# Kernel tuning notes

Hardware: AMD Instinct MI355X
Metric: run time of the kernel (lower is better)

## Reference

```python
import jax, jax.numpy as jnp
import numpy as np

B, N, DIM = 4, 2048, 1024
HEADS, DIM_HEAD = 16, 64
INNER = HEADS * DIM_HEAD


def setup_inputs() -> dict:
    key = jax.random.key(0)
    kx, kw = jax.random.split(key)
    x = jax.random.normal(kx, (B, N, DIM), dtype=jnp.float32)
    # Dense kernel [in_features, out_features], no bias
    w_qkv = jax.random.normal(kw, (DIM, 3 * INNER), dtype=jnp.float32) * (DIM ** -0.5)
    return {"x": x, "w_qkv": w_qkv}


def reference(x, w_qkv):
    scale = DIM_HEAD ** (-0.5)
    qkv = jnp.einsum('bnc,cf->bnf', x, w_qkv)  # [B, N, 3*INNER]
    q, k, v = jnp.split(qkv, 3, axis=-1)
    # 'b n (h d) -> b h n d'
    def to_heads(t):
        return t.reshape(B, N, HEADS, DIM_HEAD).transpose(0, 2, 1, 3)
    q, k, v = map(to_heads, (q, k, v))
    dots = jnp.einsum('bhid,bhjd->bhij', q, k) * scale  # [B, H, N, N]
    attn = jax.nn.softmax(dots, axis=-1)
    out = jnp.einsum('bhij,bhjd->bhid', attn, v)  # [B, H, N, D]
    # 'b h n d -> b n (h d)'
    return out.transpose(0, 2, 1, 3).reshape(B, N, INNER)
```

## Files before the change

### kernel.cpp

```cpp
#include <hip/hip_runtime.h>
#include <hip/hip_bf16.h>
#include <math.h>

typedef __bf16 bf16x2 __attribute__((ext_vector_type(2)));
typedef __bf16 bf16x4 __attribute__((ext_vector_type(4)));
typedef __bf16 bf16x8 __attribute__((ext_vector_type(8)));
typedef float f32x4 __attribute__((ext_vector_type(4)));
typedef float f32x16 __attribute__((ext_vector_type(16)));

#define MFMA16(a, b, c) __builtin_amdgcn_mfma_f32_16x16x32_bf16(a, b, c, 0, 0, 0)
#define MFMA32(a, b, c) __builtin_amdgcn_mfma_f32_32x32x16_bf16(a, b, c, 0, 0, 0)
#define QSCALE 0.1803368801111204f

__device__ __forceinline__ void gload_lds16(const __bf16* g, __bf16* l) {
  __builtin_amdgcn_global_load_lds((const __attribute__((address_space(1))) void*)g,
                                   (__attribute__((address_space(3))) void*)l,
                                   16, 0, 0);
}

__global__ __launch_bounds__(256) void convert_x(const float* __restrict__ in,
                                                 __bf16* __restrict__ out) {
  int i = blockIdx.x * 256 + threadIdx.x;
  float4 v = ((const float4*)in)[i];
  bf16x4 o = {(__bf16)v.x, (__bf16)v.y, (__bf16)v.z, (__bf16)v.w};
  *(bf16x4*)&out[i * 4] = o;
}

__global__ __launch_bounds__(256) void transpose_w(const float* __restrict__ W,
                                                   __bf16* __restrict__ Wt) {
  __shared__ __bf16 tile[64][65];
  const int bx = blockIdx.x;
  const int by = blockIdx.y;
  const int t = threadIdx.x;
  const int lr = t >> 6;
  const int lc = t & 63;
  const float sc = (bx < 16) ? QSCALE : 1.0f;
#pragma unroll
  for (int i = 0; i < 16; ++i) {
    int r = lr + i * 4;
    tile[r][lc] = (__bf16)(W[(size_t)(by * 64 + r) * 3072 + bx * 64 + lc] * sc);
  }
  __syncthreads();
#pragma unroll
  for (int i = 0; i < 16; ++i) {
    int r = lr + i * 4;
    Wt[(size_t)(bx * 64 + r) * 1024 + by * 64 + lc] = tile[lc][r];
  }
}

__global__ __launch_bounds__(256) void gemm_qkv(const __bf16* __restrict__ X,
                                                const __bf16* __restrict__ Wt,
                                                __bf16* __restrict__ QK,
                                                __bf16* __restrict__ Vt) {
  __shared__ __bf16 As[128 * 32];
  __shared__ __bf16 Bs[128 * 32];
  const int t = threadIdx.x;
  const int lane = t & 63;
  const int wave = t >> 6;
  const int quad = lane >> 4;
  const int l16 = lane & 15;
  const int n0 = blockIdx.x * 128;
  const int m0 = blockIdx.y * 128;
  const int wm = (wave & 1) * 64;
  const int wn = (wave >> 1) * 64;

  const __bf16* Ag = &X[(size_t)(m0 + wave * 16 + (lane >> 2)) * 1024 + (lane & 3) * 8];
  const __bf16* Bg = &Wt[(size_t)(n0 + wave * 16 + (lane >> 2)) * 1024 + (lane & 3) * 8];
  __bf16* As0 = &As[wave * 512];
  __bf16* As1 = &As[2048 + wave * 512];
  __bf16* Bs0 = &Bs[wave * 512];
  __bf16* Bs1 = &Bs[2048 + wave * 512];

  f32x4 acc[4][4] = {};

  for (int k0 = 0; k0 < 1024; k0 += 32) {
    gload_lds16(Ag + k0, As0);
    gload_lds16(Ag + (size_t)64 * 1024 + k0, As1);
    gload_lds16(Bg + k0, Bs0);
    gload_lds16(Bg + (size_t)64 * 1024 + k0, Bs1);
    __syncthreads();

    bf16x8 af[4], bf[4];
#pragma unroll
    for (int mi = 0; mi < 4; ++mi)
      af[mi] = *(const bf16x8*)&As[(wm + mi * 16 + l16) * 32 + quad * 8];
#pragma unroll
    for (int ni = 0; ni < 4; ++ni)
      bf[ni] = *(const bf16x8*)&Bs[(wn + ni * 16 + l16) * 32 + quad * 8];
#pragma unroll
    for (int mi = 0; mi < 4; ++mi)
#pragma unroll
      for (int ni = 0; ni < 4; ++ni)
        acc[mi][ni] = MFMA16(af[mi], bf[ni], acc[mi][ni]);
    __syncthreads();
  }

  if (n0 < 2048) {
#pragma unroll
    for (int mi = 0; mi < 4; ++mi)
#pragma unroll
      for (int ni = 0; ni < 4; ++ni)
#pragma unroll
        for (int r = 0; r < 4; ++r) {
          int row = m0 + wm + mi * 16 + quad * 4 + r;
          int col = n0 + wn + ni * 16 + l16;
          QK[(size_t)row * 2048 + col] = (__bf16)acc[mi][ni][r];
        }
  } else {
#pragma unroll
    for (int mi = 0; mi < 4; ++mi)
#pragma unroll
      for (int ni = 0; ni < 4; ++ni) {
        int v = n0 + wn + ni * 16 + l16 - 2048;
        int hh = v >> 6, d = v & 63;
        int row0 = m0 + wm + mi * 16 + quad * 4;
        int bb = row0 >> 11, key = row0 & 2047;
        bf16x4 pk = {(__bf16)acc[mi][ni][0], (__bf16)acc[mi][ni][1],
                     (__bf16)acc[mi][ni][2], (__bf16)acc[mi][ni][3]};
        *(bf16x4*)&Vt[((size_t)(bb * 16 + hh) * 64 + d) * 2048 + key] = pk;
      }
  }
}

#define AT_LD 72

__global__ __launch_bounds__(256) void attn(const __bf16* __restrict__ QK,
                                            const __bf16* __restrict__ Vt,
                                            float* __restrict__ Out) {
  const int t = threadIdx.x;
  const int lane = t & 63;
  const int wave = t >> 6;
  const int l31 = lane & 31;
  const int half = lane >> 5;

  const int flat = blockIdx.x + (blockIdx.y << 4) + (blockIdx.z << 8);
  const int xcd = flat & 7;
  const int idx = flat >> 3;
  const int bh = xcd * 8 + (idx >> 4);
  const int qb = idx & 15;
  const int b = bh >> 4;
  const int h = bh & 15;
  const int q0w = qb * 128 + wave * 32;

  const size_t base = (size_t)b * 2048 * 2048;
  const __bf16* Qb = QK + base + h * 64;
  const __bf16* Kb = QK + base + 1024 + h * 64;
  const __bf16* Vtb = Vt + (size_t)(b * 16 + h) * 64 * 2048;

  __shared__ __bf16 Ks[64 * AT_LD];
  __shared__ __bf16 Vs[64 * AT_LD];

  bf16x8 qf[4];
#pragma unroll
  for (int dc = 0; dc < 4; ++dc)
    qf[dc] = *(const bf16x8*)&Qb[(size_t)(q0w + l31) * 2048 + dc * 16 + half * 8];

  f32x16 o[2] = {};
  float lsum = 0.0f;

  const int srow = t >> 2;
  const int sc = (t & 3) * 16;
  const int prow = (srow & 51) | ((srow & 4) << 1) | ((srow & 8) >> 1);

  for (int kv0 = 0; kv0 < 2048; kv0 += 64) {
    bf16x8 k0v = *(const bf16x8*)&Kb[(size_t)(kv0 + srow) * 2048 + sc];
    bf16x8 k1v = *(const bf16x8*)&Kb[(size_t)(kv0 + srow) * 2048 + sc + 8];
    bf16x8 v0v = *(const bf16x8*)&Vtb[(size_t)srow * 2048 + kv0 + sc];
    bf16x8 v1v = *(const bf16x8*)&Vtb[(size_t)srow * 2048 + kv0 + sc + 8];
    __syncthreads();
    *(bf16x8*)&Ks[prow * AT_LD + sc] = k0v;
    *(bf16x8*)&Ks[prow * AT_LD + sc + 8] = k1v;
    *(bf16x8*)&Vs[srow * AT_LD + sc] = v0v;
    *(bf16x8*)&Vs[srow * AT_LD + sc + 8] = v1v;
    __syncthreads();

    bf16x8 pf[4];
#pragma unroll
    for (int kt = 0; kt < 2; ++kt) {
      f32x16 c = {};
#pragma unroll
      for (int dc = 0; dc < 4; ++dc) {
        bf16x8 kf = *(const bf16x8*)&Ks[(kt * 32 + l31) * AT_LD + dc * 16 + half * 8];
        c = MFMA32(kf, qf[dc], c);
      }
#pragma unroll
      for (int kkl = 0; kkl < 2; ++kkl) {
        bf16x8 f;
#pragma unroll
        for (int j = 0; j < 8; ++j) {
          float e = __builtin_amdgcn_exp2f(c[8 * kkl + 4 * (j >> 2) + (j & 3)]);
          lsum += e;
          f[j] = (__bf16)e;
        }
        pf[kt * 2 + kkl] = f;
      }
    }

#pragma unroll
    for (int dt = 0; dt < 2; ++dt)
#pragma unroll
      for (int kk = 0; kk < 4; ++kk) {
        bf16x8 vf = *(const bf16x8*)&Vs[(dt * 32 + l31) * AT_LD + kk * 16 + half * 8];
        o[dt] = MFMA32(pf[kk], vf, o[dt]);
      }
  }

  lsum += __shfl_xor(lsum, 32);
  float inv = 1.0f / lsum;

  float iv[16];
#pragma unroll
  for (int r = 0; r < 16; ++r)
    iv[r] = __shfl(inv, (r & 3) + 8 * (r >> 2) + 4 * half);

#pragma unroll
  for (int dt = 0; dt < 2; ++dt)
#pragma unroll
    for (int r = 0; r < 16; ++r) {
      int qr = (r & 3) + 8 * (r >> 2) + 4 * half;
      Out[(size_t)(b * 2048 + q0w + qr) * 1024 + h * 64 + dt * 32 + l31] =
          o[dt][r] * iv[r];
    }
}

extern "C" void kernel_launch(void* const* d_in, const int* in_sizes, int n_in,
                              void* d_out, int out_size, void* d_ws, size_t ws_size,
                              hipStream_t stream) {
  const float* x = (const float*)d_in[0];
  const float* w = (const float*)d_in[1];
  float* out = (float*)d_out;

  __bf16* Wt = (__bf16*)d_ws;
  __bf16* QK = Wt + (size_t)3072 * 1024;
  __bf16* Xb = QK + (size_t)8192 * 2048;
  __bf16* Vtr = Xb + (size_t)8192 * 1024;

  convert_x<<<8192, 256, 0, stream>>>(x, Xb);
  transpose_w<<<dim3(48, 16), 256, 0, stream>>>(w, Wt);
  gemm_qkv<<<dim3(24, 64), 256, 0, stream>>>(Xb, Wt, QK, Vtr);
  attn<<<dim3(16, 16, 4), 256, 0, stream>>>(QK, Vtr, out);
}
```

Before: 234.3 us.

## Double-buffer QKV GEMM with 256x128 tiles, swizzled LDS, interleaved loads

Rewrites the QKV projection GEMM to use 512-thread blocks with 256x128 output tiles and a K-step of 64. The LDS is double-buffered so the next tile's global-to-LDS loads are issued between MFMA groups, and only one barrier is needed per step. An XOR swizzle reduces LDS bank conflicts, and s_setprio is raised around the MFMA groups. The cost is 96KB of dynamic LDS per block, which limits occupancy, plus added scheduling complexity.

```diff
diff --git a/kernel.cpp b/kernel.cpp
--- a/kernel.cpp
+++ b/kernel.cpp
@@ -48,51 +48,125 @@
   }
 }
 
-__global__ __launch_bounds__(256) void gemm_qkv(const __bf16* __restrict__ X,
-                                                const __bf16* __restrict__ Wt,
-                                                __bf16* __restrict__ QK,
-                                                __bf16* __restrict__ Vt) {
-  __shared__ __bf16 As[128 * 32];
-  __shared__ __bf16 Bs[128 * 32];
+#define GSLOT 24576
+
+__global__ __launch_bounds__(512, 2) void gemm_qkv(const __bf16* __restrict__ X,
+                                                   const __bf16* __restrict__ Wt,
+                                                   __bf16* __restrict__ QK,
+                                                   __bf16* __restrict__ Vt) {
+  extern __shared__ __bf16 lds[];
   const int t = threadIdx.x;
   const int lane = t & 63;
-  const int wave = t >> 6;
+  const int w = t >> 6;
   const int quad = lane >> 4;
   const int l16 = lane & 15;
   const int n0 = blockIdx.x * 128;
-  const int m0 = blockIdx.y * 128;
-  const int wm = (wave & 1) * 64;
-  const int wn = (wave >> 1) * 64;
-
-  const __bf16* Ag = &X[(size_t)(m0 + wave * 16 + (lane >> 2)) * 1024 + (lane & 3) * 8];
-  const __bf16* Bg = &Wt[(size_t)(n0 + wave * 16 + (lane >> 2)) * 1024 + (lane & 3) * 8];
-  __bf16* As0 = &As[wave * 512];
-  __bf16* As1 = &As[2048 + wave * 512];
-  __bf16* Bs0 = &Bs[wave * 512];
-  __bf16* Bs1 = &Bs[2048 + wave * 512];
+  const int m0 = blockIdx.y * 256;
+  const int wm = (w >> 1) * 64;
+  const int wn = (w & 1) * 64;
+  const int sw = (lane & 12) << 2;
+  const int colSw = ((lane & 7) << 3) ^ ((lane & 32) >> 1) ^ ((w & 1) << 5);
+
+  const __bf16* Asrc = &X[(size_t)(m0 + w * 8 + (lane >> 3)) * 1024 + colSw];
+  const __bf16* Bsrc = &Wt[(size_t)(n0 + w * 8 + (lane >> 3)) * 1024 + colSw];
+  const int dstAw = w * 8 * 64;
+  const int dstBw = 16384 + w * 8 * 64;
 
   f32x4 acc[4][4] = {};
 
-  for (int k0 = 0; k0 < 1024; k0 += 32) {
-    gload_lds16(Ag + k0, As0);
-    gload_lds16(Ag + (size_t)64 * 1024 + k0, As1);
-    gload_lds16(Bg + k0, Bs0);
-    gload_lds16(Bg + (size_t)64 * 1024 + k0, Bs1);
-    __syncthreads();
-
-    bf16x8 af[4], bf[4];
-#pragma unroll
-    for (int mi = 0; mi < 4; ++mi)
-      af[mi] = *(const bf16x8*)&As[(wm + mi * 16 + l16) * 32 + quad * 8];
+  {
+    __bf16* T = lds;
+#pragma unroll
+    for (int a = 0; a < 4; ++a)
+      gload_lds16(Asrc + (size_t)a * 64 * 1024, T + dstAw + a * 4096);
+#pragma unroll
+    for (int b = 0; b < 2; ++b)
+      gload_lds16(Bsrc + (size_t)b * 64 * 1024, T + dstBw + b * 4096);
+    asm volatile("s_waitcnt vmcnt(0)" ::: "memory");
+    __builtin_amdgcn_sched_barrier(0);
+    __builtin_amdgcn_s_barrier();
+    __builtin_amdgcn_sched_barrier(0);
+  }
+
+  for (int c = 0; c < 16; ++c) {
+    __bf16* S = lds + (c & 1) * GSLOT;
+    __bf16* T = lds + ((c & 1) ^ 1) * GSLOT;
+    const size_t kn = (size_t)(c + 1) * 64;
+    const bool st = c < 15;
+
+    if (st) {
+      gload_lds16(Asrc + kn, T + dstAw);
+      gload_lds16(Asrc + (size_t)64 * 1024 + kn, T + dstAw + 4096);
+      gload_lds16(Asrc + (size_t)128 * 1024 + kn, T + dstAw + 2 * 4096);
+    }
+    bf16x8 af0[2][2], af1[2][2], bf[4][2];
+#pragma unroll
+    for (int mi = 0; mi < 2; ++mi)
+#pragma unroll
+      for (int kk = 0; kk < 2; ++kk)
+        af0[mi][kk] = *(const bf16x8*)&S[(wm + mi * 16 + l16) * 64 +
+                                         ((kk * 32 + quad * 8) ^ sw)];
 #pragma unroll
     for (int ni = 0; ni < 4; ++ni)
-      bf[ni] = *(const bf16x8*)&Bs[(wn + ni * 16 + l16) * 32 + quad * 8];
-#pragma unroll
-    for (int mi = 0; mi < 4; ++mi)
-#pragma unroll
-      for (int ni = 0; ni < 4; ++ni)
-        acc[mi][ni] = MFMA16(af[mi], bf[ni], acc[mi][ni]);
-    __syncthreads();
+#pragma unroll
+      for (int kk = 0; kk < 2; ++kk)
+        bf[ni][kk] = *(const bf16x8*)&S[16384 + (wn + ni * 16 + l16) * 64 +
+                                        ((kk * 32 + quad * 8) ^ sw)];
+    __builtin_amdgcn_s_setprio(1);
+#pragma unroll
+    for (int mi = 0; mi < 2; ++mi)
+#pragma unroll
+      for (int ni = 0; ni < 2; ++ni)
+#pragma unroll
+        for (int kk = 0; kk < 2; ++kk)
+          acc[mi][ni] = MFMA16(af0[mi][kk], bf[ni][kk], acc[mi][ni]);
+    __builtin_amdgcn_s_setprio(0);
+
+    if (st) {
+      gload_lds16(Asrc + (size_t)192 * 1024 + kn, T + dstAw + 3 * 4096);
+      gload_lds16(Bsrc + kn, T + dstBw);
+      gload_lds16(Bsrc + (size_t)64 * 1024 + kn, T + dstBw + 4096);
+    }
+    __builtin_amdgcn_s_setprio(1);
+#pragma unroll
+    for (int mi = 0; mi < 2; ++mi)
+#pragma unroll
+      for (int ni = 0; ni < 2; ++ni)
+#pragma unroll
+        for (int kk = 0; kk < 2; ++kk)
+          acc[mi][2 + ni] = MFMA16(af0[mi][kk], bf[2 + ni][kk], acc[mi][2 + ni]);
+    __builtin_amdgcn_s_setprio(0);
+
+#pragma unroll
+    for (int mi = 0; mi < 2; ++mi)
+#pragma unroll
+      for (int kk = 0; kk < 2; ++kk)
+        af1[mi][kk] = *(const bf16x8*)&S[(wm + (2 + mi) * 16 + l16) * 64 +
+                                         ((kk * 32 + quad * 8) ^ sw)];
+    __builtin_amdgcn_s_setprio(1);
+#pragma unroll
+    for (int mi = 0; mi < 2; ++mi)
+#pragma unroll
+      for (int ni = 0; ni < 2; ++ni)
+#pragma unroll
+        for (int kk = 0; kk < 2; ++kk)
+          acc[2 + mi][2 + ni] = MFMA16(af1[mi][kk], bf[2 + ni][kk], acc[2 + mi][2 + ni]);
+    __builtin_amdgcn_s_setprio(0);
+
+    __builtin_amdgcn_s_setprio(1);
+#pragma unroll
+    for (int mi = 0; mi < 2; ++mi)
+#pragma unroll
+      for (int ni = 0; ni < 2; ++ni)
+#pragma unroll
+        for (int kk = 0; kk < 2; ++kk)
+          acc[2 + mi][ni] = MFMA16(af1[mi][kk], bf[ni][kk], acc[2 + mi][ni]);
+    __builtin_amdgcn_s_setprio(0);
+
+    asm volatile("s_waitcnt vmcnt(0) lgkmcnt(0)" ::: "memory");
+    __builtin_amdgcn_sched_barrier(0);
+    __builtin_amdgcn_s_barrier();
+    __builtin_amdgcn_sched_barrier(0);
   }
 
   if (n0 < 2048) {
@@ -235,8 +309,16 @@
   __bf16* Xb = QK + (size_t)8192 * 2048;
   __bf16* Vtr = Xb + (size_t)8192 * 1024;
 
+  static bool attr_done = false;
+  if (!attr_done) {
+    (void)hipFuncSetAttribute((const void*)gemm_qkv,
+                              hipFuncAttributeMaxDynamicSharedMemorySize,
+                              2 * GSLOT * (int)sizeof(__bf16));
+    attr_done = true;
+  }
+
   convert_x<<<8192, 256, 0, stream>>>(x, Xb);
   transpose_w<<<dim3(48, 16), 256, 0, stream>>>(w, Wt);
-  gemm_qkv<<<dim3(24, 64), 256, 0, stream>>>(Xb, Wt, QK, Vtr);
+  gemm_qkv<<<dim3(24, 32), 512, 2 * GSLOT * sizeof(__bf16), stream>>>(Xb, Wt, QK, Vtr);
   attn<<<dim3(16, 16, 4), 256, 0, stream>>>(QK, Vtr, out);
 }
```

After: 239.0 us. No clear change (+2.0%).

## Pipeline QKV GEMM with 4-stage LDS ring buffer and 256x128 tiles

Applied to the files above, without the earlier changes.

Restructures the QKV projection GEMM to use 512-thread blocks computing 256x128 tiles, with a 4-deep ring of LDS buffers filled by direct global-to-LDS loads three K-steps ahead. Explicit vmcnt waits and barriers replace the per-iteration sync pairs, and MFMA sections get raised wave priority. The goal is to hide global load latency behind matrix math and improve reuse of the weight tile. It needs 96KB of dynamic LDS, which limits blocks per CU, and it relies on hand-tuned wait counts.

```diff
diff --git a/kernel.cpp b/kernel.cpp
--- a/kernel.cpp
+++ b/kernel.cpp
@@ -48,52 +48,90 @@
   }
 }
 
-__global__ __launch_bounds__(256) void gemm_qkv(const __bf16* __restrict__ X,
-                                                const __bf16* __restrict__ Wt,
-                                                __bf16* __restrict__ QK,
-                                                __bf16* __restrict__ Vt) {
-  __shared__ __bf16 As[128 * 32];
-  __shared__ __bf16 Bs[128 * 32];
+#define GTOT_B 98304
+
+__global__ __launch_bounds__(512, 2) void gemm_qkv(const __bf16* __restrict__ X,
+                                                   const __bf16* __restrict__ Wt,
+                                                   __bf16* __restrict__ QK,
+                                                   __bf16* __restrict__ Vt) {
+  extern __shared__ __bf16 lds[];
   const int t = threadIdx.x;
   const int lane = t & 63;
-  const int wave = t >> 6;
+  const int w = t >> 6;
   const int quad = lane >> 4;
   const int l16 = lane & 15;
   const int n0 = blockIdx.x * 128;
-  const int m0 = blockIdx.y * 128;
-  const int wm = (wave & 1) * 64;
-  const int wn = (wave >> 1) * 64;
-
-  const __bf16* Ag = &X[(size_t)(m0 + wave * 16 + (lane >> 2)) * 1024 + (lane & 3) * 8];
-  const __bf16* Bg = &Wt[(size_t)(n0 + wave * 16 + (lane >> 2)) * 1024 + (lane & 3) * 8];
-  __bf16* As0 = &As[wave * 512];
-  __bf16* As1 = &As[2048 + wave * 512];
-  __bf16* Bs0 = &Bs[wave * 512];
-  __bf16* Bs1 = &Bs[2048 + wave * 512];
+  const int m0 = blockIdx.y * 256;
+  const int wm = (w >> 1) * 64;
+  const int wn = (w & 1) * 64;
+
+  const __bf16* As0 = &X[(size_t)(m0 + w * 32 + (lane >> 2)) * 1024 + (lane & 3) * 8];
+  const __bf16* As1 = As0 + (size_t)16 * 1024;
+  const __bf16* Bsr = &Wt[(size_t)(n0 + w * 16 + (lane >> 2)) * 1024 + (lane & 3) * 8];
+  const int dA0 = (w * 32) * 32;
+  const int dA1 = (w * 32 + 16) * 32;
+  const int dB0 = 8192 + (w * 16) * 32;
 
   f32x4 acc[4][4] = {};
 
-  for (int k0 = 0; k0 < 1024; k0 += 32) {
-    gload_lds16(Ag + k0, As0);
-    gload_lds16(Ag + (size_t)64 * 1024 + k0, As1);
-    gload_lds16(Bg + k0, Bs0);
-    gload_lds16(Bg + (size_t)64 * 1024 + k0, Bs1);
-    __syncthreads();
-
+  auto STAGE = [&](int hh) {
+    __bf16* T = lds + (size_t)(hh & 3) * 12288;
+    const size_t kc = (size_t)hh * 32;
+    gload_lds16(As0 + kc, T + dA0);
+    gload_lds16(As1 + kc, T + dA1);
+    gload_lds16(Bsr + kc, T + dB0);
+  };
+  auto COMPUTE = [&](int hh) {
+    const __bf16* S = lds + (size_t)(hh & 3) * 12288;
     bf16x8 af[4], bf[4];
 #pragma unroll
     for (int mi = 0; mi < 4; ++mi)
-      af[mi] = *(const bf16x8*)&As[(wm + mi * 16 + l16) * 32 + quad * 8];
+      af[mi] = *(const bf16x8*)&S[(wm + mi * 16 + l16) * 32 + quad * 8];
 #pragma unroll
     for (int ni = 0; ni < 4; ++ni)
-      bf[ni] = *(const bf16x8*)&Bs[(wn + ni * 16 + l16) * 32 + quad * 8];
+      bf[ni] = *(const bf16x8*)&S[8192 + (wn + ni * 16 + l16) * 32 + quad * 8];
+    __builtin_amdgcn_s_setprio(1);
 #pragma unroll
     for (int mi = 0; mi < 4; ++mi)
 #pragma unroll
       for (int ni = 0; ni < 4; ++ni)
         acc[mi][ni] = MFMA16(af[mi], bf[ni], acc[mi][ni]);
-    __syncthreads();
-  }
+    __builtin_amdgcn_s_setprio(0);
+  };
+
+  STAGE(0);
+  STAGE(1);
+  STAGE(2);
+
+  for (int h = 0; h < 29; ++h) {
+    STAGE(h + 3);
+    asm volatile("s_waitcnt vmcnt(9)" ::: "memory");
+    __builtin_amdgcn_sched_barrier(0);
+    __builtin_amdgcn_s_barrier();
+    __builtin_amdgcn_sched_barrier(0);
+    COMPUTE(h);
+    __builtin_amdgcn_sched_barrier(0);
+    __builtin_amdgcn_s_barrier();
+  }
+  asm volatile("s_waitcnt vmcnt(6)" ::: "memory");
+  __builtin_amdgcn_sched_barrier(0);
+  __builtin_amdgcn_s_barrier();
+  __builtin_amdgcn_sched_barrier(0);
+  COMPUTE(29);
+  __builtin_amdgcn_sched_barrier(0);
+  __builtin_amdgcn_s_barrier();
+  asm volatile("s_waitcnt vmcnt(3)" ::: "memory");
+  __builtin_amdgcn_sched_barrier(0);
+  __builtin_amdgcn_s_barrier();
+  __builtin_amdgcn_sched_barrier(0);
+  COMPUTE(30);
+  __builtin_amdgcn_sched_barrier(0);
+  __builtin_amdgcn_s_barrier();
+  asm volatile("s_waitcnt vmcnt(0)" ::: "memory");
+  __builtin_amdgcn_sched_barrier(0);
+  __builtin_amdgcn_s_barrier();
+  __builtin_amdgcn_sched_barrier(0);
+  COMPUTE(31);
 
   if (n0 < 2048) {
 #pragma unroll
@@ -235,8 +273,16 @@
   __bf16* Xb = QK + (size_t)8192 * 2048;
   __bf16* Vtr = Xb + (size_t)8192 * 1024;
 
+  static bool attr_done = false;
+  if (!attr_done) {
+    (void)hipFuncSetAttribute((const void*)gemm_qkv,
+                              hipFuncAttributeMaxDynamicSharedMemorySize,
+                              GTOT_B);
+    attr_done = true;
+  }
+
   convert_x<<<8192, 256, 0, stream>>>(x, Xb);
   transpose_w<<<dim3(48, 16), 256, 0, stream>>>(w, Wt);
-  gemm_qkv<<<dim3(24, 64), 256, 0, stream>>>(Xb, Wt, QK, Vtr);
+  gemm_qkv<<<dim3(24, 32), 512, GTOT_B, stream>>>(Xb, Wt, QK, Vtr);
   attn<<<dim3(16, 16, 4), 256, 0, stream>>>(QK, Vtr, out);
 }
```

After: 245.0 us. 4.6% more time.
